# Performance work log

Measured on AMD Instinct MI355X. Metric: run time of the kernel, lower is better.

Reference implementation:

```python
import jax, jax.numpy as jnp
import numpy as np
from jax import lax

KH = KW = 3
STRIDE = (1, 1)
PAD = (1, 1)

def setup_inputs() -> dict:
    key = jax.random.key(0)
    k1, k2, k3 = jax.random.split(key, 3)
    B_, C, H, W = 16, 128, 56, 56
    O, R = 256, 16
    Kflat = C * KH * KW
    x = jax.random.normal(k1, (B_, C, H, W), dtype=jnp.float32)
    # kaiming_normal_ fan_out for A: std = sqrt(2/out_channels)
    A = jax.random.normal(k2, (O, R), dtype=jnp.float32) * np.float32(np.sqrt(2.0 / O))
    # kaiming_normal_ fan_in for B: std = sqrt(2/kernel_flat_dim)
    Bm = jax.random.normal(k3, (R, Kflat), dtype=jnp.float32) * np.float32(np.sqrt(2.0 / Kflat))
    return {"x": x, "A": A, "B": Bm}

def reference(x, A, B):
    b, c, h, w = x.shape
    h_out = (h + 2 * PAD[0] - KH) // STRIDE[0] + 1
    w_out = (w + 2 * PAD[1] - KW) // STRIDE[1] + 1
    # im2col: [B, C*KH*KW, H_out, W_out]; feature order (c, kh, kw) matches torch Unfold
    patches = lax.conv_general_dilated_patches(
        x, filter_shape=(KH, KW), window_strides=STRIDE,
        padding=((PAD[0], PAD[0]), (PAD[1], PAD[1])))
    patches = patches.reshape(b, c * KH * KW, h_out * w_out)  # [B, K, L]
    tmp = jnp.einsum('rk,bkl->brl', B, patches)               # rank-limited matmul
    out = jnp.einsum('or,brl->bol', A, tmp)                   # [B, O, L]
    return out.reshape(b, A.shape[0], h_out, w_out)
```

## Files before the change

kernel.cpp:

```cpp
#include <hip/hip_runtime.h>
#include <hip/hip_bf16.h>


#define Bn 16
#define Cc 128
#define Hh 56
#define Ww 56
#define Ll (Hh * Ww)
#define Rr 16
#define Oo 256
#define KF (Cc * 9)
#define NKS 36

typedef __attribute__((ext_vector_type(8))) short bfrag_t;
typedef __attribute__((ext_vector_type(4))) float f32x4;

__device__ __forceinline__ float bf16_bits(unsigned short u) {
    return __uint_as_float(((unsigned)u) << 16);
}

__device__ __forceinline__ unsigned short bf16_rne(float f) {
    const unsigned u = __float_as_uint(f);
    const unsigned r = u + 0x7FFFu + ((u >> 16) & 1u);
    return (unsigned short)(r >> 16);
}

__device__ __forceinline__ bool detect_bf16(const void* __restrict__ p) {
    const unsigned* w = (const unsigned*)p;
    int c = 0;
#pragma unroll
    for (int i = 0; i < 32; ++i) {
        const unsigned e = (w[i] >> 7) & 0xFFu;
        c += (e >= 96u && e <= 144u) ? 1 : 0;
    }
    return c >= 20;
}

__global__ __launch_bounds__(256) void prep_kernel(
    const void* __restrict__ A, const void* __restrict__ Bm,
    unsigned short* __restrict__ Bfrag, float* __restrict__ Afp)
{
    const bool ab = detect_bf16(A);
    const bool bb = detect_bf16(Bm);
    const int i = blockIdx.x * 256 + threadIdx.x;
    if (i < NKS * 512) {
        const int kstep = i >> 9, rem = i & 511;
        const int l = rem >> 3, e = rem & 7;
        const int r = l & 15, g = l >> 4;
        const int kp = kstep * 32 + g * 8 + e;
        const int tap = kp >> 7, c = kp & 127;
        const int k = c * 9 + tap;
        const float v = bb ? bf16_bits(((const unsigned short*)Bm)[r * KF + k])
                           : ((const float*)Bm)[r * KF + k];
        const unsigned short hi = bf16_rne(v);
        const float lov = v - bf16_bits(hi);
        Bfrag[(kstep * 2 + 0) * 512 + rem] = hi;
        Bfrag[(kstep * 2 + 1) * 512 + rem] = bf16_rne(lov);
    }
    if (i < Oo * Rr) {
        Afp[i] = ab ? bf16_bits(((const unsigned short*)A)[i])
                    : ((const float*)A)[i];
    }
}

template<bool XB>
__device__ __forceinline__ void mfma_body(
    const void* __restrict__ x,
    const unsigned short* __restrict__ Bfrag,
    const float* __restrict__ Afp,
    float* __restrict__ out,
    float (* __restrict__ tmp)[66])
{
    const int tid  = threadIdx.x;
    const int lane = tid & 63;
    const int wv   = __builtin_amdgcn_readfirstlane(tid >> 6);
    const int col  = lane & 15;
    const int g    = lane >> 4;
    const int h    = blockIdx.x;
    const int b    = blockIdx.y;
    const int px   = wv * 16 + col;

    int  off9[9];
    bool ok9[9];
#pragma unroll
    for (int dh = 0; dh < 3; ++dh) {
        const int hr = h + dh - 1;
        const bool hok = (hr >= 0) & (hr < Hh);
        const int hc = hok ? hr : (hr < 0 ? 0 : Hh - 1);
#pragma unroll
        for (int dw = 0; dw < 3; ++dw) {
            const int wr = px + dw - 1;
            const bool wok2 = (wr >= 0) & (wr < Ww);
            const int wc = wok2 ? wr : (wr < 0 ? 0 : Ww - 1);
            off9[dh * 3 + dw] = hc * Ww + wc;
            ok9[dh * 3 + dw]  = hok & wok2;
        }
    }
    unsigned cb4[4];
#pragma unroll
    for (int cb = 0; cb < 4; ++cb)
        cb4[cb] = (unsigned)((b * Cc + cb * 32 + g * 8) * Ll);

    f32x4 acc = {0.f, 0.f, 0.f, 0.f};
    const bfrag_t* __restrict__ bf = (const bfrag_t*)Bfrag;

#pragma unroll
    for (int ks = 0; ks < NKS; ++ks) {
        const int tap = ks >> 2, cb = ks & 3;
        const unsigned base = cb4[cb] + (unsigned)off9[tap];
        unsigned up[4];
#pragma unroll
        for (int j = 0; j < 4; ++j) {
            unsigned short v0, v1;
            if constexpr (XB) {
                v0 = ((const unsigned short*)x)[base + (unsigned)((2*j+0) * Ll)];
                v1 = ((const unsigned short*)x)[base + (unsigned)((2*j+1) * Ll)];
            } else {
                v0 = bf16_rne(((const float*)x)[base + (unsigned)((2*j+0) * Ll)]);
                v1 = bf16_rne(((const float*)x)[base + (unsigned)((2*j+1) * Ll)]);
            }
            const unsigned packed = (unsigned)v0 | ((unsigned)v1 << 16);
            up[j] = ok9[tap] ? packed : 0u;
        }
        union { unsigned u[4]; bfrag_t v; } pu;
        pu.u[0] = up[0]; pu.u[1] = up[1]; pu.u[2] = up[2]; pu.u[3] = up[3];
        const bfrag_t pf  = pu.v;
        const bfrag_t ahi = bf[(ks * 2 + 0) * 64 + lane];
        const bfrag_t alo = bf[(ks * 2 + 1) * 64 + lane];
        acc = __builtin_amdgcn_mfma_f32_16x16x32_bf16(ahi, pf, acc, 0, 0, 0);
        acc = __builtin_amdgcn_mfma_f32_16x16x32_bf16(alo, pf, acc, 0, 0, 0);
    }

#pragma unroll
    for (int reg = 0; reg < 4; ++reg)
        tmp[g * 4 + reg][wv * 16 + col] = acc[reg];
    __syncthreads();

    float tv[Rr];
#pragma unroll
    for (int r = 0; r < Rr; ++r) tv[r] = tmp[r][lane];

    const bool wok = (lane < Ww);
    const size_t obase = (size_t)b * Oo * Ll + (size_t)(h * Ww) + (size_t)lane;
#pragma unroll 4
    for (int j = 0; j < 64; ++j) {
        const int o = wv * 64 + j;
        const float* Ao = Afp + (size_t)o * Rr;
        float s = 0.f;
#pragma unroll
        for (int r = 0; r < Rr; ++r) s += Ao[r] * tv[r];
        if (wok) out[obase + (size_t)o * Ll] = s;
    }
}

__global__ __launch_bounds__(256, 4) void fused_mfma(
    const void* __restrict__ x,
    const unsigned short* __restrict__ Bfrag,
    const float* __restrict__ Afp,
    float* __restrict__ out)
{
    __shared__ float tmp[Rr][66];
    if (detect_bf16(x)) mfma_body<true >(x, Bfrag, Afp, out, tmp);
    else                mfma_body<false>(x, Bfrag, Afp, out, tmp);
}

__global__ __launch_bounds__(256) void fused_fallback(
    const void* __restrict__ x, const void* __restrict__ A,
    const void* __restrict__ Bm, float* __restrict__ out)
{
    const bool xb = detect_bf16(x);
    const bool ab = detect_bf16(A);
    const bool bb = detect_bf16(Bm);
    const int gid = blockIdx.x * 256 + threadIdx.x;
    const int b = gid / Ll;
    const int l = gid - b * Ll;
    const int h = l / Ww, w = l - h * Ww;
    float acc[Rr];
#pragma unroll
    for (int r = 0; r < Rr; ++r) acc[r] = 0.f;
    const size_t xbase = (size_t)b * Cc * Ll;
    for (int c = 0; c < Cc; ++c) {
        const size_t xc = xbase + (size_t)c * Ll;
        float xv[9];
#pragma unroll
        for (int dh = 0; dh < 3; ++dh) {
            const int hh = h + dh - 1;
            const bool hok = (hh >= 0) & (hh < Hh);
#pragma unroll
            for (int dw = 0; dw < 3; ++dw) {
                const int ww = w + dw - 1;
                const bool ok = hok & (ww >= 0) & (ww < Ww);
                const size_t idx = xc + (size_t)(hh * Ww + ww);
                xv[dh*3+dw] = ok ? (xb ? bf16_bits(((const unsigned short*)x)[idx])
                                       : ((const float*)x)[idx]) : 0.f;
            }
        }
#pragma unroll
        for (int r = 0; r < Rr; ++r) {
            const size_t bo = (size_t)r * KF + (size_t)c * 9;
            float s = acc[r];
#pragma unroll
            for (int i = 0; i < 9; ++i)
                s += (bb ? bf16_bits(((const unsigned short*)Bm)[bo+i])
                         : ((const float*)Bm)[bo+i]) * xv[i];
            acc[r] = s;
        }
    }
    const size_t obase = (size_t)b * Oo * Ll + (size_t)l;
    for (int o = 0; o < Oo; ++o) {
        float s = 0.f;
#pragma unroll
        for (int r = 0; r < Rr; ++r)
            s += (ab ? bf16_bits(((const unsigned short*)A)[o*Rr+r])
                     : ((const float*)A)[o*Rr+r]) * acc[r];
        out[obase + (size_t)o * Ll] = s;
    }
}

extern "C" void kernel_launch(void* const* d_in, const int* in_sizes, int n_in,
                              void* d_out, int out_size, void* d_ws, size_t ws_size,
                              hipStream_t stream) {
    const void* x  = d_in[0];
    const void* A  = d_in[1];
    const void* Bm = d_in[2];
    for (int i = 0; i < n_in && i < 3; ++i) {
        const int s = in_sizes[i];
        if      (s == Bn * Cc * Ll) x  = d_in[i];
        else if (s == Oo * Rr)      A  = d_in[i];
        else if (s == Rr * KF)      Bm = d_in[i];
    }
    float* out = (float*)d_out;

    const size_t need = (size_t)(NKS * 2 * 512) * sizeof(unsigned short)
                      + (size_t)(Oo * Rr) * sizeof(float);
    if (ws_size >= need) {
        unsigned short* Bfrag = (unsigned short*)d_ws;
        float* Afp = (float*)((char*)d_ws + (size_t)(NKS * 2 * 512) * 2);
        prep_kernel<<<dim3(72), 256, 0, stream>>>(A, Bm, Bfrag, Afp);
        fused_mfma<<<dim3(Hh, Bn), 256, 0, stream>>>(x, Bfrag, Afp, out);
    } else {
        fused_fallback<<<dim3((Bn * Ll) / 256), 256, 0, stream>>>(x, A, Bm, out);
    }
}
```

Before: 124.7 us.

## Stage swizzled input rows in LDS and compute two output rows per block

Each block now loads four padded input rows (halo included) into shared memory as bf16 in a channel-swizzled layout, then reads MFMA operands with 16-byte LDS loads instead of scattered 2-byte global gathers. Every block computes two output rows, so the B fragments are reused across rows and the halo rows are shared. The grid is halved and occupancy is lowered to 2 blocks per CU because of the larger LDS footprint. The staging phase adds a barrier and serialises load and compute within a block.

```diff
diff --git a/kernel.cpp b/kernel.cpp
--- a/kernel.cpp
+++ b/kernel.cpp
@@ -11,6 +11,10 @@
 #define Oo 256
 #define KF (Cc * 9)
 #define NKS 36
+#define W2 58
+#define RPITCH 128
+#define ROWB (W2 * RPITCH)
+#define HB 2
 
 typedef __attribute__((ext_vector_type(8))) short bfrag_t;
 typedef __attribute__((ext_vector_type(4))) float f32x4;
@@ -36,7 +40,11 @@
     return c >= 20;
 }
 
-__global__ __launch_bounds__(256) void prep_kernel(
+__device__ __forceinline__ int sw_idx(int px, int c) {
+    return px * RPITCH + (((c >> 3) ^ (px & 7)) << 3) + (c & 7);
+}
+
+__global__ __launch_bounds__(256) void prep_frag(
     const void* __restrict__ A, const void* __restrict__ Bm,
     unsigned short* __restrict__ Bfrag, float* __restrict__ Afp)
 {
@@ -64,104 +72,141 @@
 }
 
 template<bool XB>
-__device__ __forceinline__ void mfma_body(
+__device__ __forceinline__ void fused_body(
     const void* __restrict__ x,
     const unsigned short* __restrict__ Bfrag,
     const float* __restrict__ Afp,
     float* __restrict__ out,
-    float (* __restrict__ tmp)[66])
+    unsigned short* __restrict__ xs)
 {
     const int tid  = threadIdx.x;
     const int lane = tid & 63;
     const int wv   = __builtin_amdgcn_readfirstlane(tid >> 6);
     const int col  = lane & 15;
     const int g    = lane >> 4;
-    const int h    = blockIdx.x;
+    const int h0   = blockIdx.x * HB;
     const int b    = blockIdx.y;
-    const int px   = wv * 16 + col;
-
-    int  off9[9];
-    bool ok9[9];
-#pragma unroll
-    for (int dh = 0; dh < 3; ++dh) {
-        const int hr = h + dh - 1;
-        const bool hok = (hr >= 0) & (hr < Hh);
-        const int hc = hok ? hr : (hr < 0 ? 0 : Hh - 1);
-#pragma unroll
-        for (int dw = 0; dw < 3; ++dw) {
-            const int wr = px + dw - 1;
-            const bool wok2 = (wr >= 0) & (wr < Ww);
-            const int wc = wok2 ? wr : (wr < 0 ? 0 : Ww - 1);
-            off9[dh * 3 + dw] = hc * Ww + wc;
-            ok9[dh * 3 + dw]  = hok & wok2;
-        }
-    }
-    unsigned cb4[4];
-#pragma unroll
-    for (int cb = 0; cb < 4; ++cb)
-        cb4[cb] = (unsigned)((b * Cc + cb * 32 + g * 8) * Ll);
-
-    f32x4 acc = {0.f, 0.f, 0.f, 0.f};
+
+#pragma unroll
+    for (int rr = 0; rr < HB + 2; ++rr) {
+        const int hh = h0 - 1 + rr;
+        unsigned short* xr = xs + rr * ROWB;
+        if (hh >= 0 && hh < Hh) {
+#pragma unroll
+            for (int it = 0; it < 16; ++it) {
+                const int idx = it * 256 + tid;
+                const int wp = idx & 31, c = idx >> 5;
+                if (wp < 28) {
+                    unsigned short lo, hi;
+                    if constexpr (XB) {
+                        const unsigned v = ((const unsigned*)x)[
+                            (unsigned)((b * Cc + c) * (Ll / 2) + hh * (Ww / 2) + wp)];
+                        lo = (unsigned short)(v & 0xFFFFu);
+                        hi = (unsigned short)(v >> 16);
+                    } else {
+                        const unsigned base =
+                            (unsigned)((b * Cc + c) * Ll + hh * Ww + 2 * wp);
+                        lo = bf16_rne(((const float*)x)[base]);
+                        hi = bf16_rne(((const float*)x)[base + 1]);
+                    }
+                    xr[sw_idx(2 * wp + 1, c)] = lo;
+                    xr[sw_idx(2 * wp + 2, c)] = hi;
+                }
+            }
+            if (tid < 128) {
+                xr[tid] = 0;
+                xr[57 * RPITCH + tid] = 0;
+            }
+        } else {
+#pragma unroll
+            for (int it = 0; it < 15; ++it) {
+                const int idx = it * 256 + tid;
+                ((unsigned*)xr)[idx] = 0u;
+            }
+            if (tid < 3712 - 15 * 256) ((unsigned*)xr)[15 * 256 + tid] = 0u;
+        }
+    }
+    __syncthreads();
+
+    const int px  = wv * 16 + col;
+    const int pxc = px < Ww ? px : Ww - 1;
+
+    unsigned off12[12];
+#pragma unroll
+    for (int dwv = 0; dwv < 3; ++dwv) {
+#pragma unroll
+        for (int cb = 0; cb < 4; ++cb) {
+            const int p2 = pxc + dwv;
+            off12[dwv * 4 + cb] =
+                (unsigned)(p2 * RPITCH + ((((cb * 4 + g) ^ (p2 & 7))) << 3));
+        }
+    }
+
+    f32x4 acc0 = {0.f, 0.f, 0.f, 0.f};
+    f32x4 acc1 = {0.f, 0.f, 0.f, 0.f};
     const bfrag_t* __restrict__ bf = (const bfrag_t*)Bfrag;
 
 #pragma unroll
     for (int ks = 0; ks < NKS; ++ks) {
         const int tap = ks >> 2, cb = ks & 3;
-        const unsigned base = cb4[cb] + (unsigned)off9[tap];
-        unsigned up[4];
-#pragma unroll
-        for (int j = 0; j < 4; ++j) {
-            unsigned short v0, v1;
-            if constexpr (XB) {
-                v0 = ((const unsigned short*)x)[base + (unsigned)((2*j+0) * Ll)];
-                v1 = ((const unsigned short*)x)[base + (unsigned)((2*j+1) * Ll)];
-            } else {
-                v0 = bf16_rne(((const float*)x)[base + (unsigned)((2*j+0) * Ll)]);
-                v1 = bf16_rne(((const float*)x)[base + (unsigned)((2*j+1) * Ll)]);
-            }
-            const unsigned packed = (unsigned)v0 | ((unsigned)v1 << 16);
-            up[j] = ok9[tap] ? packed : 0u;
-        }
-        union { unsigned u[4]; bfrag_t v; } pu;
-        pu.u[0] = up[0]; pu.u[1] = up[1]; pu.u[2] = up[2]; pu.u[3] = up[3];
-        const bfrag_t pf  = pu.v;
+        const int dh = tap / 3, dw = tap - dh * 3;
         const bfrag_t ahi = bf[(ks * 2 + 0) * 64 + lane];
         const bfrag_t alo = bf[(ks * 2 + 1) * 64 + lane];
-        acc = __builtin_amdgcn_mfma_f32_16x16x32_bf16(ahi, pf, acc, 0, 0, 0);
-        acc = __builtin_amdgcn_mfma_f32_16x16x32_bf16(alo, pf, acc, 0, 0, 0);
-    }
-
-#pragma unroll
-    for (int reg = 0; reg < 4; ++reg)
-        tmp[g * 4 + reg][wv * 16 + col] = acc[reg];
+        const unsigned short* p0 = xs + dh * ROWB + off12[dw * 4 + cb];
+        const bfrag_t pf0 = *(const bfrag_t*)p0;
+        const bfrag_t pf1 = *(const bfrag_t*)(p0 + ROWB);
+        acc0 = __builtin_amdgcn_mfma_f32_16x16x32_bf16(ahi, pf0, acc0, 0, 0, 0);
+        acc0 = __builtin_amdgcn_mfma_f32_16x16x32_bf16(alo, pf0, acc0, 0, 0, 0);
+        acc1 = __builtin_amdgcn_mfma_f32_16x16x32_bf16(ahi, pf1, acc1, 0, 0, 0);
+        acc1 = __builtin_amdgcn_mfma_f32_16x16x32_bf16(alo, pf1, acc1, 0, 0, 0);
+    }
+
     __syncthreads();
-
-    float tv[Rr];
-#pragma unroll
-    for (int r = 0; r < Rr; ++r) tv[r] = tmp[r][lane];
+    float (*tmp)[Rr][66] = (float (*)[Rr][66])xs;
+
+#pragma unroll
+    for (int reg = 0; reg < 4; ++reg) {
+        tmp[0][g * 4 + reg][wv * 16 + col] = acc0[reg];
+        tmp[1][g * 4 + reg][wv * 16 + col] = acc1[reg];
+    }
+    __syncthreads();
+
+    float tv0[Rr], tv1[Rr];
+#pragma unroll
+    for (int r = 0; r < Rr; ++r) {
+        tv0[r] = tmp[0][r][lane];
+        tv1[r] = tmp[1][r][lane];
+    }
 
     const bool wok = (lane < Ww);
-    const size_t obase = (size_t)b * Oo * Ll + (size_t)(h * Ww) + (size_t)lane;
+    const size_t obase = (size_t)b * Oo * Ll + (size_t)(h0 * Ww) + (size_t)lane;
 #pragma unroll 4
     for (int j = 0; j < 64; ++j) {
         const int o = wv * 64 + j;
         const float* Ao = Afp + (size_t)o * Rr;
-        float s = 0.f;
-#pragma unroll
-        for (int r = 0; r < Rr; ++r) s += Ao[r] * tv[r];
-        if (wok) out[obase + (size_t)o * Ll] = s;
-    }
-}
-
-__global__ __launch_bounds__(256, 4) void fused_mfma(
+        float s0 = 0.f, s1 = 0.f;
+#pragma unroll
+        for (int r = 0; r < Rr; ++r) {
+            const float av = Ao[r];
+            s0 += av * tv0[r];
+            s1 += av * tv1[r];
+        }
+        if (wok) {
+            out[obase + (size_t)o * Ll]      = s0;
+            out[obase + (size_t)o * Ll + Ww] = s1;
+        }
+    }
+}
+
+__global__ __launch_bounds__(256, 2) void fused_one(
     const void* __restrict__ x,
     const unsigned short* __restrict__ Bfrag,
     const float* __restrict__ Afp,
     float* __restrict__ out)
 {
-    __shared__ float tmp[Rr][66];
-    if (detect_bf16(x)) mfma_body<true >(x, Bfrag, Afp, out, tmp);
-    else                mfma_body<false>(x, Bfrag, Afp, out, tmp);
+    __shared__ __align__(16) unsigned short xs[4 * ROWB];
+    if (detect_bf16(x)) fused_body<true >(x, Bfrag, Afp, out, xs);
+    else                fused_body<false>(x, Bfrag, Afp, out, xs);
 }
 
 __global__ __launch_bounds__(256) void fused_fallback(
@@ -231,13 +276,15 @@
     }
     float* out = (float*)d_out;
 
-    const size_t need = (size_t)(NKS * 2 * 512) * sizeof(unsigned short)
-                      + (size_t)(Oo * Rr) * sizeof(float);
+    const size_t frag_bytes = (size_t)(NKS * 2 * 512) * 2;
+    const size_t afp_bytes  = (size_t)(Oo * Rr) * 4;
+    const size_t need       = frag_bytes + afp_bytes;
+
     if (ws_size >= need) {
         unsigned short* Bfrag = (unsigned short*)d_ws;
-        float* Afp = (float*)((char*)d_ws + (size_t)(NKS * 2 * 512) * 2);
-        prep_kernel<<<dim3(72), 256, 0, stream>>>(A, Bm, Bfrag, Afp);
-        fused_mfma<<<dim3(Hh, Bn), 256, 0, stream>>>(x, Bfrag, Afp, out);
+        float* Afp = (float*)((char*)d_ws + frag_bytes);
+        prep_frag<<<dim3(72), 256, 0, stream>>>(A, Bm, Bfrag, Afp);
+        fused_one<<<dim3(Hh / HB, Bn), 256, 0, stream>>>(x, Bfrag, Afp, out);
     } else {
         fused_fallback<<<dim3((Bn * Ll) / 256), 256, 0, stream>>>(x, A, Bm, out);
     }
```

After: 116.4 us. -6.6%, faster.
